# Kernel optimization log

Measured on AMD Instinct MI355X. Metric: run time of the kernel, lower is better.

The kernel has to match this reference:

```python
import math
import jax, jax.numpy as jnp
import numpy as np

B, S, D, H, DFF = 2, 2048, 2048, 16, 8192
DH = D // H
EPS = 1e-5


def setup_inputs() -> dict:
    key = jax.random.key(0)
    ks = jax.random.split(key, 12)
    std = 0.02
    inp = {
        "x": jax.random.normal(ks[0], (B, S, D), dtype=jnp.float32),
        # causal mask: 1 = allowed, 0 = masked
        "attn_mask": jnp.tril(jnp.ones((S, S), dtype=jnp.int32))[None, None],
        "ln1_g": jnp.ones((D,), jnp.float32),
        "ln1_b": jnp.zeros((D,), jnp.float32),
        "wq": jax.random.normal(ks[1], (D, D), jnp.float32) * std,
        "bq": jnp.zeros((D,), jnp.float32),
        "wk": jax.random.normal(ks[2], (D, D), jnp.float32) * std,
        "bk": jnp.zeros((D,), jnp.float32),
        "wv": jax.random.normal(ks[3], (D, D), jnp.float32) * std,
        "bv": jnp.zeros((D,), jnp.float32),
        "wo": jax.random.normal(ks[4], (D, D), jnp.float32) * std,
        "bo": jnp.zeros((D,), jnp.float32),
        "ln2_g": jnp.ones((D,), jnp.float32),
        "ln2_b": jnp.zeros((D,), jnp.float32),
        "w_in": jax.random.normal(ks[5], (D, DFF), jnp.float32) * std,
        "b_in": jnp.zeros((DFF,), jnp.float32),
        "w_out": jax.random.normal(ks[6], (DFF, D), jnp.float32) * std,
        "b_out": jnp.zeros((D,), jnp.float32),
    }
    return inp


def _layernorm(x, g, b):
    m = jnp.mean(x, axis=-1, keepdims=True)
    v = jnp.mean(jnp.square(x - m), axis=-1, keepdims=True)
    return (x - m) * jax.lax.rsqrt(v + EPS) * g + b


def _block(x, attn_mask, ln1_g, ln1_b, wq, bq, wk, bk, wv, bv, wo, bo,
           ln2_g, ln2_b, w_in, b_in, w_out, b_out):
    b_, s_, d_ = x.shape
    # --- attention sublayer (pre-norm) ---
    xn = _layernorm(x, ln1_g, ln1_b)
    q = (xn @ wq + bq).reshape(b_, s_, H, DH)
    k = (xn @ wk + bk).reshape(b_, s_, H, DH)
    v = (xn @ wv + bv).reshape(b_, s_, H, DH)
    scores = jnp.einsum("bqhd,bkhd->bhqk", q, k) / math.sqrt(DH)  # [B,H,S,S]
    scores = jnp.where(attn_mask == 0, -jnp.inf, scores)
    probs = jax.nn.softmax(scores, axis=-1)
    attn = jnp.einsum("bhqk,bkhd->bqhd", probs, v).reshape(b_, s_, d_)
    x = x + (attn @ wo + bo)
    # --- MLP sublayer (pre-norm) ---
    xn = _layernorm(x, ln2_g, ln2_b)
    h = jax.nn.gelu(xn @ w_in + b_in, approximate=False)
    x = x + (h @ w_out + b_out)
    return x


def reference(x, attn_mask, ln1_g, ln1_b, wq, bq, wk, bk, wv, bv, wo, bo,
              ln2_g, ln2_b, w_in, b_in, w_out, b_out):
    return _block(x, attn_mask, ln1_g, ln1_b, wq, bq, wk, bk, wv, bv, wo, bo,
                  ln2_g, ln2_b, w_in, b_in, w_out, b_out)
```

## Files before the change

### kernel.cpp

```cpp
#include <hip/hip_runtime.h>
#include <hip/hip_bf16.h>

#define BB   2
#define SS   2048
#define DD   2048
#define HH   16
#define DHH  128
#define DFF  8192
#define MM   (BB*SS)
#define QKD  6144

typedef __hip_bfloat16 bf16;
typedef __bf16 bf16x8 __attribute__((ext_vector_type(8)));
typedef float  f32x4 __attribute__((ext_vector_type(4)));

__device__ __forceinline__ void gl2lds16(const void* g, void* lds_uniform_base) {
    __builtin_amdgcn_global_load_lds(
        (const __attribute__((address_space(1))) void*)g,
        (__attribute__((address_space(3))) void*)lds_uniform_base,
        16, 0, 0);
}

__global__ __launch_bounds__(256) void ln_kernel(const float* __restrict__ x,
                                                 const float* __restrict__ g,
                                                 const float* __restrict__ b,
                                                 bf16* __restrict__ out) {
    int row = blockIdx.x, tid = threadIdx.x;
    const float4* xr = (const float4*)(x + (size_t)row * DD);
    float4 v0 = xr[tid];
    float4 v1 = xr[tid + 256];
    float s  = v0.x + v0.y + v0.z + v0.w + v1.x + v1.y + v1.z + v1.w;
    float s2 = v0.x*v0.x + v0.y*v0.y + v0.z*v0.z + v0.w*v0.w
             + v1.x*v1.x + v1.y*v1.y + v1.z*v1.z + v1.w*v1.w;
    #pragma unroll
    for (int m = 32; m >= 1; m >>= 1) { s += __shfl_xor(s, m); s2 += __shfl_xor(s2, m); }
    __shared__ float red[8];
    int wv = tid >> 6;
    if ((tid & 63) == 0) { red[wv] = s; red[wv + 4] = s2; }
    __syncthreads();
    s  = red[0] + red[1] + red[2] + red[3];
    s2 = red[4] + red[5] + red[6] + red[7];
    float mean = s * (1.0f / DD);
    float rs = rsqrtf(s2 * (1.0f / DD) - mean * mean + 1e-5f);
    bf16* o = out + (size_t)row * DD;
    int c0 = tid * 4, c1 = (tid + 256) * 4;
    float a0[4] = {v0.x, v0.y, v0.z, v0.w};
    float a1[4] = {v1.x, v1.y, v1.z, v1.w};
    #pragma unroll
    for (int j = 0; j < 4; j++) {
        o[c0 + j] = __float2bfloat16((a0[j] - mean) * rs * g[c0 + j] + b[c0 + j]);
        o[c1 + j] = __float2bfloat16((a1[j] - mean) * rs * g[c1 + j] + b[c1 + j]);
    }
}

__global__ __launch_bounds__(256) void transpose_cast(const float* __restrict__ W,
                                                      bf16* __restrict__ Wt,
                                                      int K, int N) {
    __shared__ float t[32][33];
    int n0 = blockIdx.x * 32, k0 = blockIdx.y * 32;
    int tx = threadIdx.x, ty = threadIdx.y;
    #pragma unroll
    for (int i = 0; i < 4; i++)
        t[ty + i * 8][tx] = W[(size_t)(k0 + ty + i * 8) * N + n0 + tx];
    __syncthreads();
    #pragma unroll
    for (int i = 0; i < 4; i++)
        Wt[(size_t)(n0 + ty + i * 8) * K + k0 + tx] = __float2bfloat16(t[tx][ty + i * 8]);
}

__global__ __launch_bounds__(256) void concat3(const float* __restrict__ a,
                                               const float* __restrict__ b,
                                               const float* __restrict__ c,
                                               float* __restrict__ o) {
    int i = blockIdx.x * 256 + threadIdx.x;
    o[i] = i < 2048 ? a[i] : (i < 4096 ? b[i - 2048] : c[i - 4096]);
}

__global__ __launch_bounds__(256) void transpose_v(const bf16* __restrict__ qkv,
                                                   bf16* __restrict__ vt) {
    __shared__ bf16 t[32][33];
    int s0 = blockIdx.x * 32, d0 = blockIdx.y * 32;
    int bh = blockIdx.z;
    int b = bh >> 4, h = bh & 15;
    int tx = threadIdx.x, ty = threadIdx.y;
    #pragma unroll
    for (int i = 0; i < 4; i++)
        t[ty + i * 8][tx] = qkv[(size_t)(b * SS + s0 + ty + i * 8) * QKD + 4096 + h * DHH + d0 + tx];
    __syncthreads();
    #pragma unroll
    for (int i = 0; i < 4; i++)
        vt[(size_t)((b * HH + h) * DHH + d0 + ty + i * 8) * SS + s0 + tx] = t[tx][ty + i * 8];
}

__global__ __launch_bounds__(256) void gemm_bt(const bf16* __restrict__ A,
                                               const bf16* __restrict__ Bt,
                                               const float* __restrict__ bias,
                                               const float* __restrict__ resid,
                                               void* __restrict__ Cout,
                                               int M, int N, int K, int epi) {
    __shared__ __align__(16) bf16 As[128 * 32];
    __shared__ __align__(16) bf16 Bs[128 * 32];
    __shared__ __align__(16) float Es[4 * 16 * 68];
    int tid = threadIdx.x;
    int lane = tid & 63, wave = tid >> 6;
    int quad = lane >> 4, l15 = lane & 15;
    int wm = wave >> 1, wn = wave & 1;
    int bm0 = blockIdx.y * 128, bn0 = blockIdx.x * 128;
    const bf16* Ag = A + (size_t)bm0 * K;
    const bf16* Bg = Bt + (size_t)bn0 * K;
    f32x4 acc[4][4] = {};

    for (int kt = 0; kt < K; kt += 32) {
        __syncthreads();
        #pragma unroll
        for (int i = 0; i < 2; i++) {
            int chunk = i * 256 + tid;
            int row = chunk >> 2, c8 = chunk & 3;
            gl2lds16(Ag + (size_t)row * K + kt + c8 * 8, As + (i * 256 + wave * 64) * 8);
        }
        #pragma unroll
        for (int i = 0; i < 2; i++) {
            int chunk = i * 256 + tid;
            int row = chunk >> 2, c8 = chunk & 3;
            gl2lds16(Bg + (size_t)row * K + kt + c8 * 8, Bs + (i * 256 + wave * 64) * 8);
        }
        __syncthreads();
        bf16x8 af[4], bfr[4];
        #pragma unroll
        for (int mt = 0; mt < 4; mt++)
            af[mt] = *(const bf16x8*)(const void*)&As[(wm * 64 + mt * 16 + l15) * 32 + quad * 8];
        #pragma unroll
        for (int nt = 0; nt < 4; nt++)
            bfr[nt] = *(const bf16x8*)(const void*)&Bs[(wn * 64 + nt * 16 + l15) * 32 + quad * 8];
        #pragma unroll
        for (int mt = 0; mt < 4; mt++)
            #pragma unroll
            for (int nt = 0; nt < 4; nt++)
                acc[mt][nt] = __builtin_amdgcn_mfma_f32_16x16x32_bf16(af[mt], bfr[nt], acc[mt][nt], 0, 0, 0);
    }

    if (epi == 1) {
        #pragma unroll
        for (int nt = 0; nt < 4; nt++) {
            int col = bn0 + wn * 64 + nt * 16 + l15;
            float bv = bias[col];
            #pragma unroll
            for (int mt = 0; mt < 4; mt++)
                #pragma unroll
                for (int r = 0; r < 4; r++) {
                    int row = bm0 + wm * 64 + mt * 16 + quad * 4 + r;
                    size_t idx = (size_t)row * N + col;
                    ((float*)Cout)[idx] = acc[mt][nt][r] + bv + resid[idx];
                }
        }
    } else {
        float bv[4];
        #pragma unroll
        for (int nt = 0; nt < 4; nt++) bv[nt] = bias[bn0 + wn * 64 + nt * 16 + l15];
        int rr = lane >> 2, cc = lane & 3;
        #pragma unroll
        for (int mt = 0; mt < 4; mt++) {
            #pragma unroll
            for (int nt = 0; nt < 4; nt++)
                #pragma unroll
                for (int r = 0; r < 4; r++)
                    Es[wave * 1088 + (quad * 4 + r) * 68 + nt * 16 + l15] = acc[mt][nt][r] + bv[nt];
            asm volatile("s_waitcnt lgkmcnt(0)" ::: "memory");
            float vals[16];
            #pragma unroll
            for (int j4 = 0; j4 < 4; j4++) {
                float4 f = *(const float4*)&Es[wave * 1088 + rr * 68 + cc * 16 + j4 * 4];
                vals[j4 * 4 + 0] = f.x; vals[j4 * 4 + 1] = f.y;
                vals[j4 * 4 + 2] = f.z; vals[j4 * 4 + 3] = f.w;
            }
            asm volatile("s_waitcnt lgkmcnt(0)" ::: "memory");
            union { bf16 h[16]; uint4 u[2]; } ob;
            #pragma unroll
            for (int j = 0; j < 16; j++) {
                float v = vals[j];
                if (epi == 2) v = 0.5f * v * (1.0f + erff(v * 0.70710678118654752f));
                ob.h[j] = __float2bfloat16(v);
            }
            int grow = bm0 + wm * 64 + mt * 16 + rr;
            int gcol = bn0 + wn * 64 + cc * 16;
            uint4* dst = (uint4*)((bf16*)Cout + (size_t)grow * N + gcol);
            dst[0] = ob.u[0];
            dst[1] = ob.u[1];
        }
    }
}

__global__ __launch_bounds__(512) void flash_attn(const bf16* __restrict__ qkv,
                                                  const bf16* __restrict__ vt,
                                                  bf16* __restrict__ out) {
    __shared__ __align__(16) bf16 Qs[128 * 128];
    __shared__ __align__(16) bf16 Ks[128 * 128];
    __shared__ __align__(16) bf16 Vs[128 * 128];
    __shared__ __align__(16) bf16 Ps[8 * 16 * 128];
    int tid = threadIdx.x;
    int lane = tid & 63, wave = tid >> 6;
    int quad = lane >> 4, l15 = lane & 15;
    int xr = blockIdx.x;
    int t = (xr & 1) ? (15 - (xr >> 1)) : (xr >> 1);
    int q0 = t * 128;
    int h = blockIdx.y, b = blockIdx.z;
    int jlast = t;
    const float scale = 0.088388347648318447f;

    int srow = tid >> 4;
    int sgrp = (tid & 15) ^ (srow & 15);

    const bf16* qb = qkv + h * DHH;
    const bf16* kb = qkv + 2048 + h * DHH;

    #pragma unroll
    for (int i = 0; i < 4; i++) {
        int row = i * 32 + srow;
        gl2lds16(qb + (size_t)(b * SS + q0 + row) * QKD + sgrp * 8,
                 Qs + i * 4096 + wave * 512);
    }

    f32x4 oacc[8] = {};
    float mrun[4] = {-1e30f, -1e30f, -1e30f, -1e30f};
    float lrun[4] = {0.f, 0.f, 0.f, 0.f};

    for (int j = 0; j <= jlast; j++) {
        __syncthreads();
        #pragma unroll
        for (int i = 0; i < 4; i++) {
            int row = i * 32 + srow;
            gl2lds16(kb + (size_t)(b * SS + j * 128 + row) * QKD + sgrp * 8,
                     Ks + i * 4096 + wave * 512);
        }
        #pragma unroll
        for (int i = 0; i < 4; i++) {
            int row = i * 32 + srow;
            gl2lds16(vt + (size_t)((b * HH + h) * DHH + row) * SS + j * 128 + sgrp * 8,
                     Vs + i * 4096 + wave * 512);
        }
        __syncthreads();

        f32x4 sacc[8] = {};
        bf16x8 aq[4];
        #pragma unroll
        for (int kc = 0; kc < 4; kc++)
            aq[kc] = *(const bf16x8*)(const void*)&Qs[(wave * 16 + l15) * 128 + (((kc * 4 + quad) ^ l15) * 8)];
        #pragma unroll
        for (int n = 0; n < 8; n++)
            #pragma unroll
            for (int kc = 0; kc < 4; kc++) {
                bf16x8 bk = *(const bf16x8*)(const void*)&Ks[(n * 16 + l15) * 128 + (((kc * 4 + quad) ^ l15) * 8)];
                sacc[n] = __builtin_amdgcn_mfma_f32_16x16x32_bf16(aq[kc], bk, sacc[n], 0, 0, 0);
            }

        float mx[4] = {-1e30f, -1e30f, -1e30f, -1e30f};
        #pragma unroll
        for (int n = 0; n < 8; n++)
            #pragma unroll
            for (int r = 0; r < 4; r++) {
                float v = sacc[n][r] * scale;
                if (j == jlast) {
                    int kl = n * 16 + l15;
                    int ql = wave * 16 + quad * 4 + r;
                    if (kl > ql) v = -1e30f;
                }
                sacc[n][r] = v;
                mx[r] = fmaxf(mx[r], v);
            }
        #pragma unroll
        for (int r = 0; r < 4; r++) {
            mx[r] = fmaxf(mx[r], __shfl_xor(mx[r], 1));
            mx[r] = fmaxf(mx[r], __shfl_xor(mx[r], 2));
            mx[r] = fmaxf(mx[r], __shfl_xor(mx[r], 4));
            mx[r] = fmaxf(mx[r], __shfl_xor(mx[r], 8));
        }
        float alpha[4], rsum[4];
        #pragma unroll
        for (int r = 0; r < 4; r++) {
            float mn = fmaxf(mrun[r], mx[r]);
            alpha[r] = __expf(mrun[r] - mn);
            mrun[r] = mn;
            rsum[r] = 0.f;
        }
        #pragma unroll
        for (int n = 0; n < 8; n++)
            #pragma unroll
            for (int r = 0; r < 4; r++) {
                float p = __expf(sacc[n][r] - mrun[r]);
                sacc[n][r] = p;
                rsum[r] += p;
            }
        #pragma unroll
        for (int r = 0; r < 4; r++) {
            rsum[r] += __shfl_xor(rsum[r], 1);
            rsum[r] += __shfl_xor(rsum[r], 2);
            rsum[r] += __shfl_xor(rsum[r], 4);
            rsum[r] += __shfl_xor(rsum[r], 8);
            lrun[r] = lrun[r] * alpha[r] + rsum[r];
        }
        #pragma unroll
        for (int n = 0; n < 8; n++)
            #pragma unroll
            for (int r = 0; r < 4; r++)
                oacc[n][r] *= alpha[r];

        #pragma unroll
        for (int n = 0; n < 8; n++)
            #pragma unroll
            for (int r = 0; r < 4; r++) {
                int rowp = quad * 4 + r;
                int g = 2 * n + (l15 >> 3);
                Ps[wave * 2048 + rowp * 128 + ((g ^ rowp) * 8) + (l15 & 7)] =
                    __float2bfloat16(sacc[n][r]);
            }
        asm volatile("s_waitcnt lgkmcnt(0)" ::: "memory");

        bf16x8 ap[4];
        #pragma unroll
        for (int kc = 0; kc < 4; kc++)
            ap[kc] = *(const bf16x8*)(const void*)&Ps[wave * 2048 + l15 * 128 + (((kc * 4 + quad) ^ l15) * 8)];
        #pragma unroll
        for (int n = 0; n < 8; n++)
            #pragma unroll
            for (int kc = 0; kc < 4; kc++) {
                bf16x8 bv = *(const bf16x8*)(const void*)&Vs[(n * 16 + l15) * 128 + (((kc * 4 + quad) ^ l15) * 8)];
                oacc[n] = __builtin_amdgcn_mfma_f32_16x16x32_bf16(ap[kc], bv, oacc[n], 0, 0, 0);
            }
    }

    #pragma unroll
    for (int n = 0; n < 8; n++)
        #pragma unroll
        for (int r = 0; r < 4; r++) {
            float v = oacc[n][r] / lrun[r];
            out[(size_t)(b * SS + q0 + wave * 16 + quad * 4 + r) * DD + h * DHH + n * 16 + l15] =
                __float2bfloat16(v);
        }
}

extern "C" void kernel_launch(void* const* d_in, const int* in_sizes, int n_in,
                              void* d_out, int out_size, void* d_ws, size_t ws_size,
                              hipStream_t stream) {
    (void)in_sizes; (void)n_in; (void)out_size; (void)ws_size;
    const float* x     = (const float*)d_in[0];
    const float* ln1_g = (const float*)d_in[2];
    const float* ln1_b = (const float*)d_in[3];
    const float* wq    = (const float*)d_in[4];
    const float* bq    = (const float*)d_in[5];
    const float* wk    = (const float*)d_in[6];
    const float* bk    = (const float*)d_in[7];
    const float* wv    = (const float*)d_in[8];
    const float* bv    = (const float*)d_in[9];
    const float* wo    = (const float*)d_in[10];
    const float* bo    = (const float*)d_in[11];
    const float* ln2_g = (const float*)d_in[12];
    const float* ln2_b = (const float*)d_in[13];
    const float* w_in  = (const float*)d_in[14];
    const float* b_in  = (const float*)d_in[15];
    const float* w_out = (const float*)d_in[16];
    const float* b_out = (const float*)d_in[17];
    float* out = (float*)d_out;

    char* ws = (char*)d_ws;
    const size_t MB = 1024 * 1024;
    bf16*  wt   = (bf16*)(ws + 0 * MB);
    bf16*  xn   = (bf16*)(ws + 32 * MB);
    bf16*  qkvb = (bf16*)(ws + 48 * MB);
    bf16*  vtb  = (bf16*)(ws + 96 * MB);
    float* x1   = (float*)(ws + 112 * MB);
    float* bcat = (float*)(ws + 144 * MB);
    bf16*  hb   = (bf16*)(ws + 48 * MB);
    bf16*  att  = xn;
    bf16*  xn2  = xn;

    dim3 t256(256), t32x8(32, 8);

    ln_kernel<<<MM, t256, 0, stream>>>(x, ln1_g, ln1_b, xn);

    transpose_cast<<<dim3(DD / 32, DD / 32), t32x8, 0, stream>>>(wq, wt, DD, DD);
    transpose_cast<<<dim3(DD / 32, DD / 32), t32x8, 0, stream>>>(wk, wt + 2048 * 2048, DD, DD);
    transpose_cast<<<dim3(DD / 32, DD / 32), t32x8, 0, stream>>>(wv, wt + 2 * 2048 * 2048, DD, DD);
    concat3<<<QKD / 256, t256, 0, stream>>>(bq, bk, bv, bcat);
    gemm_bt<<<dim3(QKD / 128, MM / 128), t256, 0, stream>>>(xn, wt, bcat, nullptr, qkvb, MM, QKD, DD, 0);

    transpose_v<<<dim3(SS / 32, DHH / 32, BB * HH), t32x8, 0, stream>>>(qkvb, vtb);

    flash_attn<<<dim3(SS / 128, HH, BB), dim3(512), 0, stream>>>(qkvb, vtb, att);

    transpose_cast<<<dim3(DD / 32, DD / 32), t32x8, 0, stream>>>(wo, wt, DD, DD);
    gemm_bt<<<dim3(DD / 128, MM / 128), t256, 0, stream>>>(att, wt, bo, x, x1, MM, DD, DD, 1);

    ln_kernel<<<MM, t256, 0, stream>>>(x1, ln2_g, ln2_b, xn2);

    transpose_cast<<<dim3(DFF / 32, DD / 32), t32x8, 0, stream>>>(w_in, wt, DD, DFF);
    gemm_bt<<<dim3(DFF / 128, MM / 128), t256, 0, stream>>>(xn2, wt, b_in, nullptr, hb, MM, DFF, DD, 2);

    transpose_cast<<<dim3(DD / 32, DFF / 32), t32x8, 0, stream>>>(w_out, wt, DFF, DD);
    gemm_bt<<<dim3(DD / 128, MM / 128), t256, 0, stream>>>(hb, wt, b_out, x1, out, MM, DD, DFF, 1);
}
```

Measured before the change: 1.075 ms.

## Merge weight transposes into fused launches, share LDS, simplify GEMM addressing

Replaces six separate weight transpose/cast launches and the bias concat with two batched transpose_misc launches. The new kernel uses 64x32 tiles and writes vectorized 16-byte bf16 stores. The GEMM unions its A/B staging and epilogue LDS buffers to cut shared memory per block, which should allow higher occupancy. It also precomputes per-thread global pointers for the LDS loads. The workspace is re-laid out so all transposed weights coexist, and x1 is aliased to the output buffer; this drops the __restrict__ qualifiers and adds a sync before the epilogue reuses LDS.

```diff
diff --git a/kernel.cpp b/kernel.cpp
--- a/kernel.cpp
+++ b/kernel.cpp
@@ -53,27 +53,48 @@
     }
 }
 
-__global__ __launch_bounds__(256) void transpose_cast(const float* __restrict__ W,
-                                                      bf16* __restrict__ Wt,
-                                                      int K, int N) {
-    __shared__ float t[32][33];
-    int n0 = blockIdx.x * 32, k0 = blockIdx.y * 32;
-    int tx = threadIdx.x, ty = threadIdx.y;
-    #pragma unroll
-    for (int i = 0; i < 4; i++)
-        t[ty + i * 8][tx] = W[(size_t)(k0 + ty + i * 8) * N + n0 + tx];
+__global__ __launch_bounds__(256) void transpose_misc(int mode,
+        const float* __restrict__ wq, const float* __restrict__ wk,
+        const float* __restrict__ wv, const float* __restrict__ wo,
+        const float* __restrict__ w_in, const float* __restrict__ w_out,
+        bf16* __restrict__ wtq, bf16* __restrict__ wto,
+        bf16* __restrict__ wtin, bf16* __restrict__ wtout,
+        const float* __restrict__ bq, const float* __restrict__ bk,
+        const float* __restrict__ bv, float* __restrict__ bcat) {
+    int bid = blockIdx.x, tid = threadIdx.x;
+    const float* src;
+    bf16* dst;
+    int N, K, tile, shift;
+    if (mode == 1) {
+        src = w_out; dst = wtout; K = DFF; N = DD; tile = bid; shift = 6;
+    } else if (bid < 6144) {
+        int w = bid >> 11; tile = bid & 2047;
+        src = (w == 0) ? wq : (w == 1) ? wk : wv;
+        dst = wtq + (size_t)w * DD * DD;
+        K = DD; N = DD; shift = 6;
+    } else if (bid < 8192) {
+        src = wo; dst = wto; K = DD; N = DD; tile = bid - 6144; shift = 6;
+    } else if (bid < 16384) {
+        src = w_in; dst = wtin; K = DD; N = DFF; tile = bid - 8192; shift = 8;
+    } else {
+        int i = (bid - 16384) * 256 + tid;
+        bcat[i] = i < 2048 ? bq[i] : (i < 4096 ? bk[i - 2048] : bv[i - 4096]);
+        return;
+    }
+    int tk = tile >> shift, tn = tile & ((1 << shift) - 1);
+    int k0 = tk * 64, n0 = tn * 32;
+    __shared__ float TT[64][33];
+    int lr = tid >> 5, lc = tid & 31;
+    #pragma unroll
+    for (int p = 0; p < 8; p++)
+        TT[p * 8 + lr][lc] = src[(size_t)(k0 + p * 8 + lr) * N + n0 + lc];
     __syncthreads();
-    #pragma unroll
-    for (int i = 0; i < 4; i++)
-        Wt[(size_t)(n0 + ty + i * 8) * K + k0 + tx] = __float2bfloat16(t[tx][ty + i * 8]);
-}
-
-__global__ __launch_bounds__(256) void concat3(const float* __restrict__ a,
-                                               const float* __restrict__ b,
-                                               const float* __restrict__ c,
-                                               float* __restrict__ o) {
-    int i = blockIdx.x * 256 + threadIdx.x;
-    o[i] = i < 2048 ? a[i] : (i < 4096 ? b[i - 2048] : c[i - 4096]);
+    int ns = tid >> 3, kc = tid & 7;
+    union { bf16 h[8]; uint4 u; } ob;
+    #pragma unroll
+    for (int j = 0; j < 8; j++)
+        ob.h[j] = __float2bfloat16(TT[kc * 8 + j][ns]);
+    *(uint4*)(dst + (size_t)(n0 + ns) * K + k0 + kc * 8) = ob.u;
 }
 
 __global__ __launch_bounds__(256) void transpose_v(const bf16* __restrict__ qkv,
@@ -95,35 +116,38 @@
 __global__ __launch_bounds__(256) void gemm_bt(const bf16* __restrict__ A,
                                                const bf16* __restrict__ Bt,
                                                const float* __restrict__ bias,
-                                               const float* __restrict__ resid,
-                                               void* __restrict__ Cout,
+                                               const float* resid,
+                                               void* Cout,
                                                int M, int N, int K, int epi) {
-    __shared__ __align__(16) bf16 As[128 * 32];
-    __shared__ __align__(16) bf16 Bs[128 * 32];
-    __shared__ __align__(16) float Es[4 * 16 * 68];
+    __shared__ __align__(16) float SU[4352];
+    bf16* As = (bf16*)SU;
+    bf16* Bs = (bf16*)(SU + 2048);
+    float* Es = SU;
     int tid = threadIdx.x;
     int lane = tid & 63, wave = tid >> 6;
     int quad = lane >> 4, l15 = lane & 15;
     int wm = wave >> 1, wn = wave & 1;
     int bm0 = blockIdx.y * 128, bn0 = blockIdx.x * 128;
-    const bf16* Ag = A + (size_t)bm0 * K;
-    const bf16* Bg = Bt + (size_t)bn0 * K;
+
+    int row4 = tid >> 2, c8 = (tid & 3) * 8;
+    const bf16* a0 = A + ((size_t)bm0 + row4) * K + c8;
+    const bf16* a1 = a0 + (size_t)64 * K;
+    const bf16* b0 = Bt + ((size_t)bn0 + row4) * K + c8;
+    const bf16* b1 = b0 + (size_t)64 * K;
+    bf16* ldsA0 = As + (wave * 64) * 8;
+    bf16* ldsA1 = As + (256 + wave * 64) * 8;
+    bf16* ldsB0 = Bs + (wave * 64) * 8;
+    bf16* ldsB1 = Bs + (256 + wave * 64) * 8;
+
     f32x4 acc[4][4] = {};
 
     for (int kt = 0; kt < K; kt += 32) {
         __syncthreads();
-        #pragma unroll
-        for (int i = 0; i < 2; i++) {
-            int chunk = i * 256 + tid;
-            int row = chunk >> 2, c8 = chunk & 3;
-            gl2lds16(Ag + (size_t)row * K + kt + c8 * 8, As + (i * 256 + wave * 64) * 8);
-        }
-        #pragma unroll
-        for (int i = 0; i < 2; i++) {
-            int chunk = i * 256 + tid;
-            int row = chunk >> 2, c8 = chunk & 3;
-            gl2lds16(Bg + (size_t)row * K + kt + c8 * 8, Bs + (i * 256 + wave * 64) * 8);
-        }
+        gl2lds16(a0, ldsA0);
+        gl2lds16(a1, ldsA1);
+        gl2lds16(b0, ldsB0);
+        gl2lds16(b1, ldsB1);
+        a0 += 32; a1 += 32; b0 += 32; b1 += 32;
         __syncthreads();
         bf16x8 af[4], bfr[4];
         #pragma unroll
@@ -157,6 +181,7 @@
         float bv[4];
         #pragma unroll
         for (int nt = 0; nt < 4; nt++) bv[nt] = bias[bn0 + wn * 64 + nt * 16 + l15];
+        __syncthreads();
         int rr = lane >> 2, cc = lane & 3;
         #pragma unroll
         for (int mt = 0; mt < 4; mt++) {
@@ -363,38 +388,39 @@
 
     char* ws = (char*)d_ws;
     const size_t MB = 1024 * 1024;
-    bf16*  wt   = (bf16*)(ws + 0 * MB);
-    bf16*  xn   = (bf16*)(ws + 32 * MB);
-    bf16*  qkvb = (bf16*)(ws + 48 * MB);
-    bf16*  vtb  = (bf16*)(ws + 96 * MB);
-    float* x1   = (float*)(ws + 112 * MB);
-    float* bcat = (float*)(ws + 144 * MB);
-    bf16*  hb   = (bf16*)(ws + 48 * MB);
-    bf16*  att  = xn;
-    bf16*  xn2  = xn;
+    bf16*  wtq   = (bf16*)(ws + 0 * MB);
+    bf16*  wto   = (bf16*)(ws + 24 * MB);
+    bf16*  wtin  = (bf16*)(ws + 32 * MB);
+    bf16*  wtout = (bf16*)(ws + 0 * MB);
+    bf16*  xn    = (bf16*)(ws + 64 * MB);
+    bf16*  qkvb  = (bf16*)(ws + 80 * MB);
+    bf16*  vtb   = (bf16*)(ws + 128 * MB);
+    bf16*  hb    = (bf16*)(ws + 80 * MB);
+    float* bcat  = (float*)(ws + 144 * MB);
+    bf16*  att   = xn;
+    bf16*  xn2   = xn;
+    float* x1    = out;
 
     dim3 t256(256), t32x8(32, 8);
 
+    transpose_misc<<<16408, t256, 0, stream>>>(0, wq, wk, wv, wo, w_in, w_out,
+                                               wtq, wto, wtin, wtout, bq, bk, bv, bcat);
     ln_kernel<<<MM, t256, 0, stream>>>(x, ln1_g, ln1_b, xn);
 
-    transpose_cast<<<dim3(DD / 32, DD / 32), t32x8, 0, stream>>>(wq, wt, DD, DD);
-    transpose_cast<<<dim3(DD / 32, DD / 32), t32x8, 0, stream>>>(wk, wt + 2048 * 2048, DD, DD);
-    transpose_cast<<<dim3(DD / 32, DD / 32), t32x8, 0, stream>>>(wv, wt + 2 * 2048 * 2048, DD, DD);
-    concat3<<<QKD / 256, t256, 0, stream>>>(bq, bk, bv, bcat);
-    gemm_bt<<<dim3(QKD / 128, MM / 128), t256, 0, stream>>>(xn, wt, bcat, nullptr, qkvb, MM, QKD, DD, 0);
+    gemm_bt<<<dim3(QKD / 128, MM / 128), t256, 0, stream>>>(xn, wtq, bcat, nullptr, qkvb, MM, QKD, DD, 0);
 
     transpose_v<<<dim3(SS / 32, DHH / 32, BB * HH), t32x8, 0, stream>>>(qkvb, vtb);
 
     flash_attn<<<dim3(SS / 128, HH, BB), dim3(512), 0, stream>>>(qkvb, vtb, att);
 
-    transpose_cast<<<dim3(DD / 32, DD / 32), t32x8, 0, stream>>>(wo, wt, DD, DD);
-    gemm_bt<<<dim3(DD / 128, MM / 128), t256, 0, stream>>>(att, wt, bo, x, x1, MM, DD, DD, 1);
+    gemm_bt<<<dim3(DD / 128, MM / 128), t256, 0, stream>>>(att, wto, bo, x, x1, MM, DD, DD, 1);
+
+    transpose_misc<<<8192, t256, 0, stream>>>(1, wq, wk, wv, wo, w_in, w_out,
+                                              wtq, wto, wtin, wtout, bq, bk, bv, bcat);
 
     ln_kernel<<<MM, t256, 0, stream>>>(x1, ln2_g, ln2_b, xn2);
 
-    transpose_cast<<<dim3(DFF / 32, DD / 32), t32x8, 0, stream>>>(w_in, wt, DD, DFF);
-    gemm_bt<<<dim3(DFF / 128, MM / 128), t256, 0, stream>>>(xn2, wt, b_in, nullptr, hb, MM, DFF, DD, 2);
-
-    transpose_cast<<<dim3(DD / 32, DFF / 32), t32x8, 0, stream>>>(w_out, wt, DFF, DD);
-    gemm_bt<<<dim3(DD / 128, MM / 128), t256, 0, stream>>>(hb, wt, b_out, x1, out, MM, DD, DFF, 1);
-}
+    gemm_bt<<<dim3(DFF / 128, MM / 128), t256, 0, stream>>>(xn2, wtin, b_in, nullptr, hb, MM, DFF, DD, 2);
+
+    gemm_bt<<<dim3(DD / 128, MM / 128), t256, 0, stream>>>(hb, wtout, b_out, x1, out, MM, DD, DFF, 1);
+}
```

Result: slower. 1.101 ms (+2.5%).
